# Optimization experiments

Hardware: AMD Instinct MI355X
Metric: run time of the kernel (lower is better)

The kernel has to match this reference:

```python
import jax, jax.numpy as jnp
import numpy as np

B, N, C, H = 8192, 36, 128, 8
HD = C // H  # 16
FOCUS = 3
EPS = 1e-4


def setup_inputs() -> dict:
    key = jax.random.key(0)
    ks = jax.random.split(key, 10)
    x = jax.random.normal(ks[0], (B, N, C), dtype=jnp.float32)
    pos = jax.random.normal(ks[1], (B, N, C), dtype=jnp.float32)
    mask = jax.random.randint(ks[2], (B, N), 0, 2).astype(jnp.float32)
    coords = jax.random.randint(ks[3], (B * N, 4), 0, 8).astype(jnp.int64)
    voxel_inds = jax.random.permutation(ks[4], B * N).reshape(B, N).astype(jnp.int64)
    s = 0.02
    qk_w = jax.random.normal(ks[5], (C, 2 * C), dtype=jnp.float32) * s
    qk_b = jnp.zeros((2 * C,), dtype=jnp.float32)
    v_w = jax.random.normal(ks[6], (C, C), dtype=jnp.float32) * s
    v_b = jnp.zeros((C,), dtype=jnp.float32)
    proj_w = jax.random.normal(ks[7], (C, C), dtype=jnp.float32) * s
    proj_b = jnp.zeros((C,), dtype=jnp.float32)
    return {"x": x, "pos": pos, "mask": mask, "qk_w": qk_w, "qk_b": qk_b,
            "v_w": v_w, "v_b": v_b, "proj_w": proj_w, "proj_b": proj_b,
            "coords": coords, "voxel_inds": voxel_inds}


def reference(x, pos, mask, qk_w, qk_b, v_w, v_b, proj_w, proj_b, coords, voxel_inds):
    b, n, c = x.shape
    qk = (x + pos) @ qk_w + qk_b                      # (B,N,2C)
    q, k = qk[..., :c], qk[..., c:]
    v = x @ v_w + v_b                                 # (B,N,C)
    k = k * mask[..., None]
    # split heads -> (B,H,N,HD)
    q = q.reshape(b, n, H, HD).transpose(0, 2, 1, 3)
    k = k.reshape(b, n, H, HD).transpose(0, 2, 1, 3)
    v = v.reshape(b, n, H, HD).transpose(0, 2, 1, 3)
    # focusing power
    q = q ** FOCUS
    k = k ** FOCUS
    # q normalized per-token over channels; k normalized per-channel over tokens
    # (original rearranges k to (bh, c, n) before norm(dim=-1))
    q = q / (EPS + jnp.linalg.norm(q, axis=-1, keepdims=True))
    k = k / (EPS + jnp.linalg.norm(k, axis=2, keepdims=True))
    # linear attention: kv = k^T v (HD x HD), then q @ kv
    kv = jnp.einsum('bhnc,bhnd->bhcd', k, v)          # (B,H,HD,HD)
    out = jnp.einsum('bhnc,bhcd->bhnd', q, kv)        # (B,H,N,HD)
    out = out.transpose(0, 2, 1, 3).reshape(b, n, c)  # (B,N,C)
    num = jnp.sum(mask, axis=-1, keepdims=True)       # (B,1)
    out = out / (num[..., None] + EPS)
    # inverse-permutation gather: perm[voxel_inds.flat] = arange
    flat = voxel_inds.reshape(-1)
    M = coords.shape[0]
    perm = jnp.zeros((M,), dtype=flat.dtype).at[flat].set(
        jnp.arange(M, dtype=flat.dtype))
    out = out.reshape(-1, c)[perm]                    # (M,C)
    out = out @ proj_w + proj_b
    return out
```

## Files before the change

### kernel.cpp

```cpp
#include <hip/hip_runtime.h>

typedef __bf16 bf16x8 __attribute__((ext_vector_type(8)));
typedef float f32x4 __attribute__((ext_vector_type(4)));

#define Bdim 8192
#define Nn 36
#define Cc 128
#define EPSf 1e-4f

#define WS_QK_HI 0
#define WS_QK_LO 32768
#define WS_V_HI  65536
#define WS_P_HI  81920

#define OFF_XH   0
#define OFF_PH   12288
#define OFF_PL   24576
#define OFF_KT   0
#define OFF_VT   12288
#define OFF_QH   24576
#define OFF_KV   33792
#define OFF_O    0
#define OFF_MASK 39936
#define OFF_VOX  40128
#define OFF_INN  40272
#define LDS_BYTES 40448

__device__ inline uint bfh(float f) {
    __bf16 h = (__bf16)f;
    return (uint)(*(const ushort*)&h);
}
__device__ inline uint bfl(float f) {
    float hf = (float)((__bf16)f);
    __bf16 l = (__bf16)(f - hf);
    return (uint)(*(const ushort*)&l);
}
__device__ inline uint pk2h(float a, float b) { return bfh(a) | (bfh(b) << 16); }
__device__ inline uint pk2l(float a, float b) { return bfl(a) | (bfl(b) << 16); }

union U8 { bf16x8 v; uint u[4]; };

__global__ __launch_bounds__(256)
void prep_frags(const float* __restrict__ qk_w, const float* __restrict__ v_w,
                const float* __restrict__ proj_w, ushort* __restrict__ ws)
{
    int e = blockIdx.x * 256 + threadIdx.x;
    const float* W; int N; int idx; int hi_off; int lo_off;
    if (e < 32768)      { W = qk_w;   N = 256; hi_off = WS_QK_HI; lo_off = WS_QK_LO; idx = e; }
    else if (e < 49152) { W = v_w;    N = 128; hi_off = WS_V_HI;  lo_off = -1;       idx = e - 32768; }
    else                { W = proj_w; N = 128; hi_off = WS_P_HI;  lo_off = -1;       idx = e - 49152; }
    int j    = idx & 7;
    int lane = (idx >> 3) & 63;
    int ks   = (idx >> 9) & 3;
    int ct   = idx >> 11;
    int col  = ct * 16 + (lane & 15);
    int k    = ks * 32 + (lane >> 4) * 8 + j;
    float v  = W[k * N + col];
    ws[hi_off + idx] = (ushort)bfh(v);
    if (lo_off >= 0) ws[lo_off + idx] = (ushort)bfl(v);
}

__global__ __launch_bounds__(512, 6)
void fla_mfma(const float* __restrict__ x, const float* __restrict__ pos,
              const float* __restrict__ mask, const float* __restrict__ qk_b,
              const float* __restrict__ v_b, const float* __restrict__ proj_b,
              const int* __restrict__ vox, const ushort* __restrict__ ws,
              float* __restrict__ out)
{
    __shared__ __align__(16) char lds[LDS_BYTES];
    const int t = threadIdx.x;
    const int b = blockIdx.x;
    const int lane = t & 63;
    const int wv = t >> 6;

    const int  rsel = lane & 15;
    const int  grp  = lane >> 4;
    const uint kgrp = (uint)grp * 8u;
    const uint sw   = ((uint)rsel) << 4;

    const float* xg = x + (size_t)b * (Nn * Cc);
    const float* pg = pos + (size_t)b * (Nn * Cc);
    #pragma unroll
    for (int it = 0; it < 3; ++it) {
        int idx = t + it * 512;
        int n = idx >> 5;
        int c4 = (idx & 31) << 2;
        float4 xv = make_float4(0.f, 0.f, 0.f, 0.f);
        float4 pv = make_float4(0.f, 0.f, 0.f, 0.f);
        if (n < Nn) {
            xv = *(const float4*)(xg + n * Cc + c4);
            pv = *(const float4*)(pg + n * Cc + c4);
        }
        float s0 = xv.x + pv.x, s1 = xv.y + pv.y, s2 = xv.z + pv.z, s3 = xv.w + pv.w;
        uint ba = (uint)n * 256u + (((uint)(c4 * 2)) ^ (((uint)n & 15u) << 4));
        *(uint2*)(lds + OFF_XH + ba) = make_uint2(pk2h(xv.x, xv.y), pk2h(xv.z, xv.w));
        *(uint2*)(lds + OFF_PH + ba) = make_uint2(pk2h(s0, s1), pk2h(s2, s3));
        *(uint2*)(lds + OFF_PL + ba) = make_uint2(pk2l(s0, s1), pk2l(s2, s3));
    }
    if (t < 48) ((float*)(lds + OFF_MASK))[t] = (t < Nn) ? mask[(size_t)b * Nn + t] : 0.f;
    if (t >= 64 && t < 64 + Nn) ((int*)(lds + OFF_VOX))[t - 64] = vox[(size_t)b * Nn + (t - 64)];
    if (t == 128) {
        float s = 0.f;
        for (int n = 0; n < Nn; ++n) s += mask[(size_t)b * Nn + n];
        *(float*)(lds + OFF_INN) = 1.f / (s + EPSf);
    }
    __syncthreads();

    f32x4 accV[3];
    f32x4 accQ[3][2];
    #pragma unroll
    for (int rt = 0; rt < 3; ++rt) {
        accV[rt] = (f32x4){0.f, 0.f, 0.f, 0.f};
        accQ[rt][0] = (f32x4){0.f, 0.f, 0.f, 0.f};
        accQ[rt][1] = (f32x4){0.f, 0.f, 0.f, 0.f};
    }
    #pragma unroll
    for (int ks = 0; ks < 4; ++ks) {
        uint ka = (((uint)(ks * 32) + kgrp) * 2u) ^ sw;
        bf16x8 xh[3];
        #pragma unroll
        for (int rt = 0; rt < 3; ++rt)
            xh[rt] = *(const bf16x8*)(lds + OFF_XH + (uint)(rt * 16 + rsel) * 256u + ka);
        int f = ((wv * 4 + ks) * 64 + lane) * 8;
        bf16x8 bvh = *(const bf16x8*)(ws + WS_V_HI + f);
        #pragma unroll
        for (int rt = 0; rt < 3; ++rt)
            accV[rt] = __builtin_amdgcn_mfma_f32_16x16x32_bf16(xh[rt], bvh, accV[rt], 0, 0, 0);
    }
    #pragma unroll
    for (int ks = 0; ks < 4; ++ks) {
        uint ka = (((uint)(ks * 32) + kgrp) * 2u) ^ sw;
        bf16x8 ph[3], pl[3];
        #pragma unroll
        for (int rt = 0; rt < 3; ++rt) {
            uint ba = (uint)(rt * 16 + rsel) * 256u + ka;
            ph[rt] = *(const bf16x8*)(lds + OFF_PH + ba);
            pl[rt] = *(const bf16x8*)(lds + OFF_PL + ba);
        }
        #pragma unroll
        for (int ci = 0; ci < 2; ++ci) {
            int f = (((wv * 2 + ci) * 4 + ks) * 64 + lane) * 8;
            bf16x8 bh = *(const bf16x8*)(ws + WS_QK_HI + f);
            bf16x8 bl = *(const bf16x8*)(ws + WS_QK_LO + f);
            #pragma unroll
            for (int rt = 0; rt < 3; ++rt) {
                accQ[rt][ci] = __builtin_amdgcn_mfma_f32_16x16x32_bf16(ph[rt], bh, accQ[rt][ci], 0, 0, 0);
                accQ[rt][ci] = __builtin_amdgcn_mfma_f32_16x16x32_bf16(ph[rt], bl, accQ[rt][ci], 0, 0, 0);
                accQ[rt][ci] = __builtin_amdgcn_mfma_f32_16x16x32_bf16(pl[rt], bh, accQ[rt][ci], 0, 0, 0);
            }
        }
    }
    __syncthreads();

    const float* sM = (const float*)(lds + OFF_MASK);
    {
        int colv = wv * 16 + rsel;
        float vb = v_b[colv];
        #pragma unroll
        for (int rt = 0; rt < 3; ++rt) {
            float a0 = accV[rt][0] + vb, a1 = accV[rt][1] + vb;
            float a2 = accV[rt][2] + vb, a3 = accV[rt][3] + vb;
            uint addr = OFF_VT + (uint)(colv * 48 + rt * 16 + grp * 4) * 2u;
            *(uint2*)(lds + addr) = make_uint2(pk2h(a0, a1), pk2h(a2, a3));
        }
    }
    if (wv < 4) {
        #pragma unroll
        for (int ci = 0; ci < 2; ++ci) {
            int colq = (wv * 2 + ci) * 16 + rsel;
            float qb = qk_b[colq];
            uint cb2 = (uint)(colq * 2);
            #pragma unroll
            for (int rt = 0; rt < 3; ++rt) {
                #pragma unroll
                for (int r = 0; r < 4; ++r) {
                    int row = rt * 16 + grp * 4 + r;
                    if (row < Nn) {
                        float q1 = accQ[rt][ci][r] + qb;
                        float q3 = q1 * q1 * q1;
                        uint ba = (uint)row * 256u + (cb2 ^ (((uint)row & 15u) << 4));
                        *(ushort*)(lds + OFF_QH + ba) = (ushort)bfh(q3);
                    }
                }
            }
        }
    } else {
        #pragma unroll
        for (int ci = 0; ci < 2; ++ci) {
            int colk = ((wv - 4) * 2 + ci) * 16 + rsel;
            float kb = qk_b[Cc + colk];
            #pragma unroll
            for (int rt = 0; rt < 3; ++rt) {
                float k3v[4];
                #pragma unroll
                for (int r = 0; r < 4; ++r) {
                    int row = rt * 16 + grp * 4 + r;
                    float k1 = (accQ[rt][ci][r] + kb) * sM[row];
                    k3v[r] = k1 * k1 * k1;
                }
                uint addr = OFF_KT + (uint)(colk * 48 + rt * 16 + grp * 4) * 2u;
                *(uint2*)(lds + addr) = make_uint2(pk2h(k3v[0], k3v[1]), pk2h(k3v[2], k3v[3]));
            }
        }
    }
    __syncthreads();

    {
        int col16 = wv * 16 + rsel;
        uint a0 = OFF_KT + (uint)(col16 * 48 + grp * 8) * 2u;
        uint b0 = OFF_VT + (uint)(col16 * 48 + grp * 8) * 2u;
        bf16x8 kA0 = *(const bf16x8*)(lds + a0);
        bf16x8 vB0 = *(const bf16x8*)(lds + b0);
        U8 kA1, vB1;
        kA1.u[0] = kA1.u[1] = kA1.u[2] = kA1.u[3] = 0u;
        vB1.u[0] = vB1.u[1] = vB1.u[2] = vB1.u[3] = 0u;
        if (grp < 2) {
            kA1.v = *(const bf16x8*)(lds + a0 + 64);
            vB1.v = *(const bf16x8*)(lds + b0 + 64);
        }
        float s = 0.f;
        #pragma unroll
        for (int j = 0; j < 8; ++j) { float q = (float)kA0[j]; s += q * q; }
        #pragma unroll
        for (int j = 0; j < 8; ++j) { float q = (float)kA1.v[j]; s += q * q; }
        s += __shfl_xor(s, 16);
        s += __shfl_xor(s, 32);
        float invkn = 1.f / (EPSf + sqrtf(s));

        f32x4 kvacc = (f32x4){0.f, 0.f, 0.f, 0.f};
        kvacc = __builtin_amdgcn_mfma_f32_16x16x32_bf16(kA0, vB0, kvacc, 0, 0, 0);
        kvacc = __builtin_amdgcn_mfma_f32_16x16x32_bf16(kA1.v, vB1.v, kvacc, 0, 0, 0);

        float f0 = __shfl(invkn, grp * 4 + 0);
        float f1 = __shfl(invkn, grp * 4 + 1);
        float f2 = __shfl(invkn, grp * 4 + 2);
        float f3 = __shfl(invkn, grp * 4 + 3);
        uint addr = OFF_KV + (uint)(wv * 384 + rsel * 24 + grp * 4) * 2u;
        *(uint2*)(lds + addr) =
            make_uint2(pk2h(kvacc[0] * f0, kvacc[1] * f1), pk2h(kvacc[2] * f2, kvacc[3] * f3));
    }
    __syncthreads();

    {
        int d = rsel;
        float inn = *(const float*)(lds + OFF_INN);
        U8 bkv;
        bkv.u[0] = bkv.u[1] = bkv.u[2] = bkv.u[3] = 0u;
        if (grp < 2)
            bkv.v = *(const bf16x8*)(lds + OFF_KV + (uint)(wv * 384 + d * 24 + grp * 8) * 2u);
        f32x4 oacc[3];
        float invn[3];
        #pragma unroll
        for (int rt = 0; rt < 3; ++rt) {
            int row = rt * 16 + rsel;
            U8 aq;
            aq.u[0] = aq.u[1] = aq.u[2] = aq.u[3] = 0u;
            if (grp < 2 && row < Nn) {
                uint ba = (uint)row * 256u +
                          (((uint)((wv * 16 + grp * 8) * 2)) ^ (((uint)row & 15u) << 4));
                aq.v = *(const bf16x8*)(lds + OFF_QH + ba);
            }
            float s = 0.f;
            #pragma unroll
            for (int j = 0; j < 8; ++j) { float q = (float)aq.v[j]; s += q * q; }
            s += __shfl_xor(s, 16);
            invn[rt] = 1.f / (EPSf + sqrtf(s));
            f32x4 o = (f32x4){0.f, 0.f, 0.f, 0.f};
            o = __builtin_amdgcn_mfma_f32_16x16x32_bf16(aq.v, bkv.v, o, 0, 0, 0);
            oacc[rt] = o;
        }
        #pragma unroll
        for (int rt = 0; rt < 3; ++rt) {
            #pragma unroll
            for (int r = 0; r < 4; ++r) {
                int rr = grp * 4 + r;
                int row = rt * 16 + rr;
                float fac = __shfl(invn[rt], rr) * inn;
                float val = oacc[rt][r] * fac;
                uint ba = (uint)row * 256u +
                          (((uint)((wv * 16 + d) * 2)) ^ (((uint)row & 15u) << 4));
                *(ushort*)(lds + OFF_O + ba) = (ushort)bfh(val);
            }
        }
    }
    __syncthreads();

    f32x4 accP[3];
    #pragma unroll
    for (int rt = 0; rt < 3; ++rt) accP[rt] = (f32x4){0.f, 0.f, 0.f, 0.f};
    #pragma unroll
    for (int ks = 0; ks < 4; ++ks) {
        uint ka = (((uint)(ks * 32) + kgrp) * 2u) ^ sw;
        bf16x8 oa[3];
        #pragma unroll
        for (int rt = 0; rt < 3; ++rt)
            oa[rt] = *(const bf16x8*)(lds + OFF_O + (uint)(rt * 16 + rsel) * 256u + ka);
        int f = ((wv * 4 + ks) * 64 + lane) * 8;
        bf16x8 bp = *(const bf16x8*)(ws + WS_P_HI + f);
        #pragma unroll
        for (int rt = 0; rt < 3; ++rt)
            accP[rt] = __builtin_amdgcn_mfma_f32_16x16x32_bf16(oa[rt], bp, accP[rt], 0, 0, 0);
    }
    {
        const int* sVx = (const int*)(lds + OFF_VOX);
        int col = wv * 16 + rsel;
        float pb = proj_b[col];
        #pragma unroll
        for (int rt = 0; rt < 3; ++rt) {
            #pragma unroll
            for (int r = 0; r < 4; ++r) {
                int row = rt * 16 + grp * 4 + r;
                if (row < Nn)
                    out[(size_t)sVx[row] * Cc + col] = accP[rt][r] + pb;
            }
        }
    }
}

extern "C" void kernel_launch(void* const* d_in, const int* in_sizes, int n_in,
                              void* d_out, int out_size, void* d_ws, size_t ws_size,
                              hipStream_t stream) {
    (void)in_sizes; (void)n_in; (void)out_size; (void)ws_size;
    const float* x      = (const float*)d_in[0];
    const float* pos    = (const float*)d_in[1];
    const float* mask   = (const float*)d_in[2];
    const float* qk_w   = (const float*)d_in[3];
    const float* qk_b   = (const float*)d_in[4];
    const float* v_w    = (const float*)d_in[5];
    const float* v_b    = (const float*)d_in[6];
    const float* proj_w = (const float*)d_in[7];
    const float* proj_b = (const float*)d_in[8];
    const int*   vox    = (const int*)d_in[10];
    ushort* ws = (ushort*)d_ws;
    float* outp = (float*)d_out;

    hipLaunchKernelGGL(prep_frags, dim3(256), dim3(256), 0, stream, qk_w, v_w, proj_w, ws);
    hipLaunchKernelGGL(fla_mfma, dim3(Bdim), dim3(512), 0, stream,
                       x, pos, mask, qk_b, v_b, proj_b, vox, ws, outp);
}
```

Baseline: 218.9 us.

## Make blocks persistent over 16 batches with double-buffered LDS prefetch

Each block now handles 16 batch elements in a loop instead of one. The next element's x/pos/mask/vox are loaded into registers during the current element's GEMMs and written into a second LDS buffer at the end of the iteration, so global load latency overlaps compute. The kv stage now builds the q@kv operand with shuffles instead of going through LDS, which removes one barrier. The K/V transposed layout is padded and its tail rows are zeroed. LDS use doubles and the launch bound drops to 4 blocks per CU, and the grid shrinks to 512 blocks, so occupancy and load balance could suffer.

```diff
diff --git a/kernel.cpp b/kernel.cpp
--- a/kernel.cpp
+++ b/kernel.cpp
@@ -4,6 +4,8 @@
 typedef float f32x4 __attribute__((ext_vector_type(4)));
 
 #define Bdim 8192
+#define NBATCH 16
+#define NBLK (Bdim / NBATCH)
 #define Nn 36
 #define Cc 128
 #define EPSf 1e-4f
@@ -17,14 +19,12 @@
 #define OFF_PH   12288
 #define OFF_PL   24576
 #define OFF_KT   0
-#define OFF_VT   12288
-#define OFF_QH   24576
-#define OFF_KV   33792
-#define OFF_O    0
+#define OFF_VT   13312
+#define OFF_QO   27648
 #define OFF_MASK 39936
 #define OFF_VOX  40128
 #define OFF_INN  40272
-#define LDS_BYTES 40448
+#define AST      40448
 
 __device__ inline uint bfh(float f) {
     __bf16 h = (__bf16)f;
@@ -60,260 +60,309 @@
     if (lo_off >= 0) ws[lo_off + idx] = (ushort)bfl(v);
 }
 
-__global__ __launch_bounds__(512, 6)
+__global__ __launch_bounds__(512, 4)
 void fla_mfma(const float* __restrict__ x, const float* __restrict__ pos,
               const float* __restrict__ mask, const float* __restrict__ qk_b,
               const float* __restrict__ v_b, const float* __restrict__ proj_b,
               const int* __restrict__ vox, const ushort* __restrict__ ws,
               float* __restrict__ out)
 {
-    __shared__ __align__(16) char lds[LDS_BYTES];
+    __shared__ __align__(16) char lds[2][AST];
     const int t = threadIdx.x;
-    const int b = blockIdx.x;
     const int lane = t & 63;
     const int wv = t >> 6;
-
     const int  rsel = lane & 15;
     const int  grp  = lane >> 4;
     const uint kgrp = (uint)grp * 8u;
     const uint sw   = ((uint)rsel) << 4;
 
-    const float* xg = x + (size_t)b * (Nn * Cc);
-    const float* pg = pos + (size_t)b * (Nn * Cc);
-    #pragma unroll
-    for (int it = 0; it < 3; ++it) {
-        int idx = t + it * 512;
-        int n = idx >> 5;
-        int c4 = (idx & 31) << 2;
-        float4 xv = make_float4(0.f, 0.f, 0.f, 0.f);
-        float4 pv = make_float4(0.f, 0.f, 0.f, 0.f);
-        if (n < Nn) {
-            xv = *(const float4*)(xg + n * Cc + c4);
-            pv = *(const float4*)(pg + n * Cc + c4);
-        }
-        float s0 = xv.x + pv.x, s1 = xv.y + pv.y, s2 = xv.z + pv.z, s3 = xv.w + pv.w;
-        uint ba = (uint)n * 256u + (((uint)(c4 * 2)) ^ (((uint)n & 15u) << 4));
-        *(uint2*)(lds + OFF_XH + ba) = make_uint2(pk2h(xv.x, xv.y), pk2h(xv.z, xv.w));
-        *(uint2*)(lds + OFF_PH + ba) = make_uint2(pk2h(s0, s1), pk2h(s2, s3));
-        *(uint2*)(lds + OFF_PL + ba) = make_uint2(pk2l(s0, s1), pk2l(s2, s3));
-    }
-    if (t < 48) ((float*)(lds + OFF_MASK))[t] = (t < Nn) ? mask[(size_t)b * Nn + t] : 0.f;
-    if (t >= 64 && t < 64 + Nn) ((int*)(lds + OFF_VOX))[t - 64] = vox[(size_t)b * Nn + (t - 64)];
-    if (t == 128) {
-        float s = 0.f;
-        for (int n = 0; n < Nn; ++n) s += mask[(size_t)b * Nn + n];
-        *(float*)(lds + OFF_INN) = 1.f / (s + EPSf);
-    }
+    const int base = blockIdx.x * NBATCH;
+
+    float4 sx0, sx1, sx2, sp0, sp1, sp2;
+    float  mv = 0.f;
+    int    vx = 0;
+
+    auto stage_load = [&](int bb) {
+        const float* xg = x + (size_t)bb * (Nn * Cc);
+        const float* pg = pos + (size_t)bb * (Nn * Cc);
+        {
+            int n = t >> 5, c4 = (t & 31) << 2;
+            sx0 = *(const float4*)(xg + n * Cc + c4);
+            sp0 = *(const float4*)(pg + n * Cc + c4);
+        }
+        {
+            int idx = t + 512;
+            int n = idx >> 5, c4 = (idx & 31) << 2;
+            sx1 = *(const float4*)(xg + n * Cc + c4);
+            sp1 = *(const float4*)(pg + n * Cc + c4);
+        }
+        if (t < 128) {
+            int idx = t + 1024;
+            int n = idx >> 5, c4 = (idx & 31) << 2;
+            sx2 = *(const float4*)(xg + n * Cc + c4);
+            sp2 = *(const float4*)(pg + n * Cc + c4);
+        }
+        mv = 0.f;
+        if (t < Nn) mv = mask[(size_t)bb * Nn + t];
+        if (t >= 64 && t < 64 + Nn) vx = vox[(size_t)bb * Nn + (t - 64)];
+    };
+
+    auto stage_write = [&](char* L) {
+        auto put = [&](int idx, float4 xv, float4 pv) {
+            int n = idx >> 5, c4 = (idx & 31) << 2;
+            float s0 = xv.x + pv.x, s1 = xv.y + pv.y;
+            float s2 = xv.z + pv.z, s3 = xv.w + pv.w;
+            uint ba = (uint)n * 256u + (((uint)(c4 * 2)) ^ (((uint)n & 15u) << 4));
+            *(uint2*)(L + OFF_XH + ba) = make_uint2(pk2h(xv.x, xv.y), pk2h(xv.z, xv.w));
+            *(uint2*)(L + OFF_PH + ba) = make_uint2(pk2h(s0, s1), pk2h(s2, s3));
+            *(uint2*)(L + OFF_PL + ba) = make_uint2(pk2l(s0, s1), pk2l(s2, s3));
+        };
+        put(t, sx0, sp0);
+        put(t + 512, sx1, sp1);
+        if (t < 128) put(t + 1024, sx2, sp2);
+        if (t < 48) ((float*)(L + OFF_MASK))[t] = (t < Nn) ? mv : 0.f;
+        if (t >= 64 && t < 64 + Nn) ((int*)(L + OFF_VOX))[t - 64] = vx;
+        if (wv == 0) {
+            float s = mv;
+            s += __shfl_xor(s, 1);  s += __shfl_xor(s, 2);
+            s += __shfl_xor(s, 4);  s += __shfl_xor(s, 8);
+            s += __shfl_xor(s, 16); s += __shfl_xor(s, 32);
+            if (lane == 0) *(float*)(L + OFF_INN) = 1.f / (s + EPSf);
+        }
+    };
+
+    stage_load(base);
+    stage_write(lds[0]);
     __syncthreads();
 
-    f32x4 accV[3];
-    f32x4 accQ[3][2];
-    #pragma unroll
-    for (int rt = 0; rt < 3; ++rt) {
-        accV[rt] = (f32x4){0.f, 0.f, 0.f, 0.f};
-        accQ[rt][0] = (f32x4){0.f, 0.f, 0.f, 0.f};
-        accQ[rt][1] = (f32x4){0.f, 0.f, 0.f, 0.f};
-    }
-    #pragma unroll
-    for (int ks = 0; ks < 4; ++ks) {
-        uint ka = (((uint)(ks * 32) + kgrp) * 2u) ^ sw;
-        bf16x8 xh[3];
-        #pragma unroll
-        for (int rt = 0; rt < 3; ++rt)
-            xh[rt] = *(const bf16x8*)(lds + OFF_XH + (uint)(rt * 16 + rsel) * 256u + ka);
-        int f = ((wv * 4 + ks) * 64 + lane) * 8;
-        bf16x8 bvh = *(const bf16x8*)(ws + WS_V_HI + f);
-        #pragma unroll
-        for (int rt = 0; rt < 3; ++rt)
-            accV[rt] = __builtin_amdgcn_mfma_f32_16x16x32_bf16(xh[rt], bvh, accV[rt], 0, 0, 0);
-    }
-    #pragma unroll
-    for (int ks = 0; ks < 4; ++ks) {
-        uint ka = (((uint)(ks * 32) + kgrp) * 2u) ^ sw;
-        bf16x8 ph[3], pl[3];
+    #pragma unroll 2
+    for (int i = 0; i < NBATCH; ++i) {
+        char* L  = lds[i & 1];
+        char* Ln = lds[(i + 1) & 1];
+
+        f32x4 accQ[3][2];
+        f32x4 accV[3];
         #pragma unroll
         for (int rt = 0; rt < 3; ++rt) {
-            uint ba = (uint)(rt * 16 + rsel) * 256u + ka;
-            ph[rt] = *(const bf16x8*)(lds + OFF_PH + ba);
-            pl[rt] = *(const bf16x8*)(lds + OFF_PL + ba);
+            accV[rt] = (f32x4){0.f, 0.f, 0.f, 0.f};
+            accQ[rt][0] = (f32x4){0.f, 0.f, 0.f, 0.f};
+            accQ[rt][1] = (f32x4){0.f, 0.f, 0.f, 0.f};
         }
         #pragma unroll
-        for (int ci = 0; ci < 2; ++ci) {
-            int f = (((wv * 2 + ci) * 4 + ks) * 64 + lane) * 8;
-            bf16x8 bh = *(const bf16x8*)(ws + WS_QK_HI + f);
-            bf16x8 bl = *(const bf16x8*)(ws + WS_QK_LO + f);
-            #pragma unroll
-            for (int rt = 0; rt < 3; ++rt) {
-                accQ[rt][ci] = __builtin_amdgcn_mfma_f32_16x16x32_bf16(ph[rt], bh, accQ[rt][ci], 0, 0, 0);
-                accQ[rt][ci] = __builtin_amdgcn_mfma_f32_16x16x32_bf16(ph[rt], bl, accQ[rt][ci], 0, 0, 0);
-                accQ[rt][ci] = __builtin_amdgcn_mfma_f32_16x16x32_bf16(pl[rt], bh, accQ[rt][ci], 0, 0, 0);
-            }
-        }
-    }
-    __syncthreads();
-
-    const float* sM = (const float*)(lds + OFF_MASK);
-    {
-        int colv = wv * 16 + rsel;
-        float vb = v_b[colv];
+        for (int ks = 0; ks < 4; ++ks) {
+            uint ka = (((uint)(ks * 32) + kgrp) * 2u) ^ sw;
+            bf16x8 xh[3];
+            #pragma unroll
+            for (int rt = 0; rt < 3; ++rt)
+                xh[rt] = *(const bf16x8*)(L + OFF_XH + (uint)(rt * 16 + rsel) * 256u + ka);
+            int f = ((wv * 4 + ks) * 64 + lane) * 8;
+            bf16x8 bvh = *(const bf16x8*)(ws + WS_V_HI + f);
+            #pragma unroll
+            for (int rt = 0; rt < 3; ++rt)
+                accV[rt] = __builtin_amdgcn_mfma_f32_16x16x32_bf16(xh[rt], bvh, accV[rt], 0, 0, 0);
+        }
         #pragma unroll
-        for (int rt = 0; rt < 3; ++rt) {
-            float a0 = accV[rt][0] + vb, a1 = accV[rt][1] + vb;
-            float a2 = accV[rt][2] + vb, a3 = accV[rt][3] + vb;
-            uint addr = OFF_VT + (uint)(colv * 48 + rt * 16 + grp * 4) * 2u;
-            *(uint2*)(lds + addr) = make_uint2(pk2h(a0, a1), pk2h(a2, a3));
-        }
-    }
-    if (wv < 4) {
-        #pragma unroll
-        for (int ci = 0; ci < 2; ++ci) {
-            int colq = (wv * 2 + ci) * 16 + rsel;
-            float qb = qk_b[colq];
-            uint cb2 = (uint)(colq * 2);
+        for (int ks = 0; ks < 4; ++ks) {
+            uint ka = (((uint)(ks * 32) + kgrp) * 2u) ^ sw;
+            bf16x8 ph[3], pl[3];
+            #pragma unroll
+            for (int rt = 0; rt < 3; ++rt) {
+                uint ba = (uint)(rt * 16 + rsel) * 256u + ka;
+                ph[rt] = *(const bf16x8*)(L + OFF_PH + ba);
+                pl[rt] = *(const bf16x8*)(L + OFF_PL + ba);
+            }
+            #pragma unroll
+            for (int ci = 0; ci < 2; ++ci) {
+                int f = (((wv * 2 + ci) * 4 + ks) * 64 + lane) * 8;
+                bf16x8 bh = *(const bf16x8*)(ws + WS_QK_HI + f);
+                bf16x8 bl = *(const bf16x8*)(ws + WS_QK_LO + f);
+                #pragma unroll
+                for (int rt = 0; rt < 3; ++rt) {
+                    accQ[rt][ci] = __builtin_amdgcn_mfma_f32_16x16x32_bf16(ph[rt], bh, accQ[rt][ci], 0, 0, 0);
+                    accQ[rt][ci] = __builtin_amdgcn_mfma_f32_16x16x32_bf16(ph[rt], bl, accQ[rt][ci], 0, 0, 0);
+                    accQ[rt][ci] = __builtin_amdgcn_mfma_f32_16x16x32_bf16(pl[rt], bh, accQ[rt][ci], 0, 0, 0);
+                }
+            }
+        }
+        if (i + 1 < NBATCH) stage_load(base + i + 1);
+        __syncthreads();
+
+        {
+            const float* sM = (const float*)(L + OFF_MASK);
+            {
+                int colv = wv * 16 + rsel;
+                float vb = v_b[colv];
+                #pragma unroll
+                for (int rt = 0; rt < 3; ++rt) {
+                    float a0 = accV[rt][0] + vb, a1 = accV[rt][1] + vb;
+                    float a2 = accV[rt][2] + vb, a3 = accV[rt][3] + vb;
+                    if (rt == 2 && grp != 0) { a0 = 0.f; a1 = 0.f; a2 = 0.f; a3 = 0.f; }
+                    uint addr = OFF_VT + (uint)(colv * 52 + rt * 16 + grp * 4) * 2u;
+                    *(uint2*)(L + addr) = make_uint2(pk2h(a0, a1), pk2h(a2, a3));
+                }
+            }
+            if (wv < 4) {
+                #pragma unroll
+                for (int ci = 0; ci < 2; ++ci) {
+                    int colq = (wv * 2 + ci) * 16 + rsel;
+                    float qb = qk_b[colq];
+                    uint cb2 = (uint)(colq * 2);
+                    #pragma unroll
+                    for (int rt = 0; rt < 3; ++rt) {
+                        #pragma unroll
+                        for (int r = 0; r < 4; ++r) {
+                            int row = rt * 16 + grp * 4 + r;
+                            if (row < Nn) {
+                                float q1 = accQ[rt][ci][r] + qb;
+                                float q3 = q1 * q1 * q1;
+                                uint ba = (uint)row * 256u + (cb2 ^ (((uint)row & 15u) << 4));
+                                *(ushort*)(L + OFF_QO + ba) = (ushort)bfh(q3);
+                            }
+                        }
+                    }
+                }
+            } else {
+                #pragma unroll
+                for (int ci = 0; ci < 2; ++ci) {
+                    int colk = ((wv - 4) * 2 + ci) * 16 + rsel;
+                    float kb = qk_b[Cc + colk];
+                    #pragma unroll
+                    for (int rt = 0; rt < 3; ++rt) {
+                        float k3v[4];
+                        #pragma unroll
+                        for (int r = 0; r < 4; ++r) {
+                            int row = rt * 16 + grp * 4 + r;
+                            float k1 = (accQ[rt][ci][r] + kb) * sM[row];
+                            float k3 = k1 * k1 * k1;
+                            k3v[r] = (rt == 2 && grp != 0) ? 0.f : k3;
+                        }
+                        uint addr = OFF_KT + (uint)(colk * 52 + rt * 16 + grp * 4) * 2u;
+                        *(uint2*)(L + addr) = make_uint2(pk2h(k3v[0], k3v[1]), pk2h(k3v[2], k3v[3]));
+                    }
+                }
+            }
+        }
+        __syncthreads();
+
+        {
+            uint bkvU[4];
+            {
+                int col16 = wv * 16 + rsel;
+                uint a0 = OFF_KT + (uint)(col16 * 52 + grp * 8) * 2u;
+                uint b0 = OFF_VT + (uint)(col16 * 52 + grp * 8) * 2u;
+                bf16x8 kA0 = *(const bf16x8*)(L + a0);
+                bf16x8 vB0 = *(const bf16x8*)(L + b0);
+                U8 kA1, vB1;
+                kA1.u[0] = kA1.u[1] = kA1.u[2] = kA1.u[3] = 0u;
+                vB1.u[0] = vB1.u[1] = vB1.u[2] = vB1.u[3] = 0u;
+                if (grp < 2) {
+                    kA1.v = *(const bf16x8*)(L + a0 + 64);
+                    vB1.v = *(const bf16x8*)(L + b0 + 64);
+                }
+                float s = 0.f;
+                #pragma unroll
+                for (int j = 0; j < 8; ++j) { float q = (float)kA0[j]; s += q * q; }
+                #pragma unroll
+                for (int j = 0; j < 8; ++j) { float q = (float)kA1.v[j]; s += q * q; }
+                s += __shfl_xor(s, 16);
+                s += __shfl_xor(s, 32);
+                float invkn = 1.f / (EPSf + sqrtf(s));
+
+                f32x4 kvacc = (f32x4){0.f, 0.f, 0.f, 0.f};
+                kvacc = __builtin_amdgcn_mfma_f32_16x16x32_bf16(kA0, vB0, kvacc, 0, 0, 0);
+                kvacc = __builtin_amdgcn_mfma_f32_16x16x32_bf16(kA1.v, vB1.v, kvacc, 0, 0, 0);
+                #pragma unroll
+                for (int r = 0; r < 4; ++r)
+                    kvacc[r] *= __shfl(invkn, grp * 4 + r);
+
+                float bv[8];
+                #pragma unroll
+                for (int j = 0; j < 8; ++j)
+                    bv[j] = __shfl(kvacc[j & 3], rsel + 16 * (2 * grp + (j >> 2)));
+                if (grp >= 2) {
+                    #pragma unroll
+                    for (int j = 0; j < 8; ++j) bv[j] = 0.f;
+                }
+                bkvU[0] = pk2h(bv[0], bv[1]);
+                bkvU[1] = pk2h(bv[2], bv[3]);
+                bkvU[2] = pk2h(bv[4], bv[5]);
+                bkvU[3] = pk2h(bv[6], bv[7]);
+            }
+            float inn = *(const float*)(L + OFF_INN);
+            U8 aq[3];
+            uint cb = (uint)(wv * 32 + grp * 16);
+            #pragma unroll
+            for (int rt = 0; rt < 3; ++rt) {
+                int row = rt * 16 + rsel;
+                aq[rt].u[0] = aq[rt].u[1] = aq[rt].u[2] = aq[rt].u[3] = 0u;
+                if (grp < 2 && row < Nn)
+                    aq[rt].v = *(const bf16x8*)(L + OFF_QO + (uint)row * 256u + (cb ^ sw));
+            }
+            f32x4 oacc[3];
+            float invn[3];
+            U8 bkv;
+            bkv.u[0] = bkvU[0]; bkv.u[1] = bkvU[1]; bkv.u[2] = bkvU[2]; bkv.u[3] = bkvU[3];
+            #pragma unroll
+            for (int rt = 0; rt < 3; ++rt) {
+                float s = 0.f;
+                #pragma unroll
+                for (int j = 0; j < 8; ++j) { float q = (float)aq[rt].v[j]; s += q * q; }
+                s += __shfl_xor(s, 16);
+                invn[rt] = 1.f / (EPSf + sqrtf(s));
+                f32x4 o = (f32x4){0.f, 0.f, 0.f, 0.f};
+                o = __builtin_amdgcn_mfma_f32_16x16x32_bf16(aq[rt].v, bkv.v, o, 0, 0, 0);
+                oacc[rt] = o;
+            }
+            uint cb2 = (uint)((wv * 16 + rsel) * 2);
+            #pragma unroll
+            for (int rt = 0; rt < 3; ++rt) {
+                #pragma unroll
+                for (int r = 0; r < 4; ++r) {
+                    int rr = grp * 4 + r;
+                    int row = rt * 16 + rr;
+                    if (row < Nn) {
+                        float fac = __shfl(invn[rt], rr) * inn;
+                        float val = oacc[rt][r] * fac;
+                        uint ba = (uint)row * 256u + (cb2 ^ (((uint)row & 15u) << 4));
+                        *(ushort*)(L + OFF_QO + ba) = (ushort)bfh(val);
+                    }
+                }
+            }
+        }
+        __syncthreads();
+
+        {
+            f32x4 accP[3];
+            #pragma unroll
+            for (int rt = 0; rt < 3; ++rt) accP[rt] = (f32x4){0.f, 0.f, 0.f, 0.f};
+            #pragma unroll
+            for (int ks = 0; ks < 4; ++ks) {
+                uint ka = (((uint)(ks * 32) + kgrp) * 2u) ^ sw;
+                bf16x8 oa[3];
+                #pragma unroll
+                for (int rt = 0; rt < 3; ++rt)
+                    oa[rt] = *(const bf16x8*)(L + OFF_QO + (uint)(rt * 16 + rsel) * 256u + ka);
+                int f = ((wv * 4 + ks) * 64 + lane) * 8;
+                bf16x8 bp = *(const bf16x8*)(ws + WS_P_HI + f);
+                #pragma unroll
+                for (int rt = 0; rt < 3; ++rt)
+                    accP[rt] = __builtin_amdgcn_mfma_f32_16x16x32_bf16(oa[rt], bp, accP[rt], 0, 0, 0);
+            }
+            const int* sVx = (const int*)(L + OFF_VOX);
+            int col = wv * 16 + rsel;
+            float pb = proj_b[col];
             #pragma unroll
             for (int rt = 0; rt < 3; ++rt) {
                 #pragma unroll
                 for (int r = 0; r < 4; ++r) {
                     int row = rt * 16 + grp * 4 + r;
-                    if (row < Nn) {
-                        float q1 = accQ[rt][ci][r] + qb;
-                        float q3 = q1 * q1 * q1;
-                        uint ba = (uint)row * 256u + (cb2 ^ (((uint)row & 15u) << 4));
-                        *(ushort*)(lds + OFF_QH + ba) = (ushort)bfh(q3);
-                    }
-                }
-            }
-        }
-    } else {
-        #pragma unroll
-        for (int ci = 0; ci < 2; ++ci) {
-            int colk = ((wv - 4) * 2 + ci) * 16 + rsel;
-            float kb = qk_b[Cc + colk];
-            #pragma unroll
-            for (int rt = 0; rt < 3; ++rt) {
-                float k3v[4];
-                #pragma unroll
-                for (int r = 0; r < 4; ++r) {
-                    int row = rt * 16 + grp * 4 + r;
-                    float k1 = (accQ[rt][ci][r] + kb) * sM[row];
-                    k3v[r] = k1 * k1 * k1;
-                }
-                uint addr = OFF_KT + (uint)(colk * 48 + rt * 16 + grp * 4) * 2u;
-                *(uint2*)(lds + addr) = make_uint2(pk2h(k3v[0], k3v[1]), pk2h(k3v[2], k3v[3]));
-            }
-        }
-    }
-    __syncthreads();
-
-    {
-        int col16 = wv * 16 + rsel;
-        uint a0 = OFF_KT + (uint)(col16 * 48 + grp * 8) * 2u;
-        uint b0 = OFF_VT + (uint)(col16 * 48 + grp * 8) * 2u;
-        bf16x8 kA0 = *(const bf16x8*)(lds + a0);
-        bf16x8 vB0 = *(const bf16x8*)(lds + b0);
-        U8 kA1, vB1;
-        kA1.u[0] = kA1.u[1] = kA1.u[2] = kA1.u[3] = 0u;
-        vB1.u[0] = vB1.u[1] = vB1.u[2] = vB1.u[3] = 0u;
-        if (grp < 2) {
-            kA1.v = *(const bf16x8*)(lds + a0 + 64);
-            vB1.v = *(const bf16x8*)(lds + b0 + 64);
-        }
-        float s = 0.f;
-        #pragma unroll
-        for (int j = 0; j < 8; ++j) { float q = (float)kA0[j]; s += q * q; }
-        #pragma unroll
-        for (int j = 0; j < 8; ++j) { float q = (float)kA1.v[j]; s += q * q; }
-        s += __shfl_xor(s, 16);
-        s += __shfl_xor(s, 32);
-        float invkn = 1.f / (EPSf + sqrtf(s));
-
-        f32x4 kvacc = (f32x4){0.f, 0.f, 0.f, 0.f};
-        kvacc = __builtin_amdgcn_mfma_f32_16x16x32_bf16(kA0, vB0, kvacc, 0, 0, 0);
-        kvacc = __builtin_amdgcn_mfma_f32_16x16x32_bf16(kA1.v, vB1.v, kvacc, 0, 0, 0);
-
-        float f0 = __shfl(invkn, grp * 4 + 0);
-        float f1 = __shfl(invkn, grp * 4 + 1);
-        float f2 = __shfl(invkn, grp * 4 + 2);
-        float f3 = __shfl(invkn, grp * 4 + 3);
-        uint addr = OFF_KV + (uint)(wv * 384 + rsel * 24 + grp * 4) * 2u;
-        *(uint2*)(lds + addr) =
-            make_uint2(pk2h(kvacc[0] * f0, kvacc[1] * f1), pk2h(kvacc[2] * f2, kvacc[3] * f3));
-    }
-    __syncthreads();
-
-    {
-        int d = rsel;
-        float inn = *(const float*)(lds + OFF_INN);
-        U8 bkv;
-        bkv.u[0] = bkv.u[1] = bkv.u[2] = bkv.u[3] = 0u;
-        if (grp < 2)
-            bkv.v = *(const bf16x8*)(lds + OFF_KV + (uint)(wv * 384 + d * 24 + grp * 8) * 2u);
-        f32x4 oacc[3];
-        float invn[3];
-        #pragma unroll
-        for (int rt = 0; rt < 3; ++rt) {
-            int row = rt * 16 + rsel;
-            U8 aq;
-            aq.u[0] = aq.u[1] = aq.u[2] = aq.u[3] = 0u;
-            if (grp < 2 && row < Nn) {
-                uint ba = (uint)row * 256u +
-                          (((uint)((wv * 16 + grp * 8) * 2)) ^ (((uint)row & 15u) << 4));
-                aq.v = *(const bf16x8*)(lds + OFF_QH + ba);
-            }
-            float s = 0.f;
-            #pragma unroll
-            for (int j = 0; j < 8; ++j) { float q = (float)aq.v[j]; s += q * q; }
-            s += __shfl_xor(s, 16);
-            invn[rt] = 1.f / (EPSf + sqrtf(s));
-            f32x4 o = (f32x4){0.f, 0.f, 0.f, 0.f};
-            o = __builtin_amdgcn_mfma_f32_16x16x32_bf16(aq.v, bkv.v, o, 0, 0, 0);
-            oacc[rt] = o;
-        }
-        #pragma unroll
-        for (int rt = 0; rt < 3; ++rt) {
-            #pragma unroll
-            for (int r = 0; r < 4; ++r) {
-                int rr = grp * 4 + r;
-                int row = rt * 16 + rr;
-                float fac = __shfl(invn[rt], rr) * inn;
-                float val = oacc[rt][r] * fac;
-                uint ba = (uint)row * 256u +
-                          (((uint)((wv * 16 + d) * 2)) ^ (((uint)row & 15u) << 4));
-                *(ushort*)(lds + OFF_O + ba) = (ushort)bfh(val);
-            }
-        }
-    }
-    __syncthreads();
-
-    f32x4 accP[3];
-    #pragma unroll
-    for (int rt = 0; rt < 3; ++rt) accP[rt] = (f32x4){0.f, 0.f, 0.f, 0.f};
-    #pragma unroll
-    for (int ks = 0; ks < 4; ++ks) {
-        uint ka = (((uint)(ks * 32) + kgrp) * 2u) ^ sw;
-        bf16x8 oa[3];
-        #pragma unroll
-        for (int rt = 0; rt < 3; ++rt)
-            oa[rt] = *(const bf16x8*)(lds + OFF_O + (uint)(rt * 16 + rsel) * 256u + ka);
-        int f = ((wv * 4 + ks) * 64 + lane) * 8;
-        bf16x8 bp = *(const bf16x8*)(ws + WS_P_HI + f);
-        #pragma unroll
-        for (int rt = 0; rt < 3; ++rt)
-            accP[rt] = __builtin_amdgcn_mfma_f32_16x16x32_bf16(oa[rt], bp, accP[rt], 0, 0, 0);
-    }
-    {
-        const int* sVx = (const int*)(lds + OFF_VOX);
-        int col = wv * 16 + rsel;
-        float pb = proj_b[col];
-        #pragma unroll
-        for (int rt = 0; rt < 3; ++rt) {
-            #pragma unroll
-            for (int r = 0; r < 4; ++r) {
-                int row = rt * 16 + grp * 4 + r;
-                if (row < Nn)
-                    out[(size_t)sVx[row] * Cc + col] = accP[rt][r] + pb;
-            }
-        }
+                    if (row < Nn)
+                        out[(size_t)sVx[row] * Cc + col] = accP[rt][r] + pb;
+                }
+            }
+        }
+        if (i + 1 < NBATCH) stage_write(Ln);
+        __syncthreads();
     }
 }
 
@@ -335,6 +384,6 @@
     float* outp = (float*)d_out;
 
     hipLaunchKernelGGL(prep_frags, dim3(256), dim3(256), 0, stream, qk_w, v_w, proj_w, ws);
-    hipLaunchKernelGGL(fla_mfma, dim3(Bdim), dim3(512), 0, stream,
+    hipLaunchKernelGGL(fla_mfma, dim3(NBLK), dim3(512), 0, stream,
                        x, pos, mask, qk_b, v_b, proj_b, vox, ws, outp);
 }
```

Measured after the change: 529.0 us. +141.7%, slower.
